# Performance work log

Hardware: AMD Instinct MI355X
Metric: run time of the kernel (lower is better)

The kernel has to match this reference:

```python
import jax, jax.numpy as jnp
import numpy as np

DIM = 512      # model dim
HEADS = 8      # attention heads
WS = 256       # window_size
G = 32         # num_global_tokens
SPARSITY = 0.3 # fraction of entries masked out per row by the sparsity controller


def setup_inputs() -> dict:
    key = jax.random.key(0)
    ks = jax.random.split(key, 7)
    b, n = 4, 8192
    x = jax.random.normal(ks[0], (b, n, DIM), dtype=jnp.float32)
    w_qkv = jax.random.normal(ks[1], (DIM, 3 * DIM), dtype=jnp.float32) * (DIM ** -0.5)
    w_out = jax.random.normal(ks[2], (DIM, DIM), dtype=jnp.float32) * (DIM ** -0.5)
    b_out = jnp.zeros((DIM,), dtype=jnp.float32)
    local_bias = jax.random.normal(ks[3], (HEADS, WS, WS), dtype=jnp.float32)
    global_param = jax.random.normal(ks[4], (HEADS, G, WS), dtype=jnp.float32)
    gate = jax.random.normal(ks[5], (HEADS,), dtype=jnp.float32)
    return {"x": x, "w_qkv": w_qkv, "w_out": w_out, "b_out": b_out,
            "local_bias": local_bias, "global_param": global_param, "gate": gate}


def reference(x, w_qkv, w_out, b_out, local_bias, global_param, gate):
    b, n, _ = x.shape
    h, ws, g = HEADS, WS, G
    d = DIM // h
    w = n // ws  # number of windows
    scale = DIM ** -0.5

    qkv = x @ w_qkv                      # [b, n, 3*dim]
    q, k, v = jnp.split(qkv, 3, axis=-1)

    def to_win(t):  # [b, n, dim] -> [b, h, w, ws, d]
        return t.reshape(b, n, h, d).transpose(0, 2, 1, 3).reshape(b, h, w, ws, d)

    q, k, v = to_win(q), to_win(k), to_win(v)

    # windowed local attention with learned per-window additive bias
    local = jnp.einsum('bhwnd,bhwmd->bhwnm', q, k) * scale   # [b,h,w,ws,ws]
    local = local + local_bias[None, :, None]                # bias broadcast over b, w

    # global-token attention term built from window-averaged q/k
    q_mean = q.mean(axis=2)  # [b,h,ws,d]
    k_mean = k.mean(axis=2)  # [b,h,ws,d]
    global_q = jnp.einsum('hgn,bhnd->bhgd', global_param, q_mean)      # [b,h,g,d]
    global_scores = jnp.einsum('bhgd,bhmd->bhgm', global_q, k_mean) * scale  # [b,h,g,ws]
    global_bias = global_scores.mean(axis=2)                            # [b,h,ws]

    # sparsity controller: learned per-head gate combines local + global,
    # then top-k row sparsification keeps (1-sparsity) of entries pre-softmax
    gate_h = jax.nn.sigmoid(gate)[None, :, None, None, None]
    scores = local + gate_h * global_bias[:, :, None, None, :]          # [b,h,w,ws,ws]
    k_keep = int(ws * (1.0 - SPARSITY))
    thresh = jax.lax.top_k(scores, k_keep)[0][..., -1:]                 # kth largest per row
    scores = jnp.where(scores >= thresh, scores, jnp.float32(-1e9))

    attn = jax.nn.softmax(scores, axis=-1)
    out = jnp.einsum('bhwnm,bhwmd->bhwnd', attn, v)                     # [b,h,w,ws,d]
    out = out.reshape(b, h, n, d).transpose(0, 2, 1, 3).reshape(b, n, DIM)
    return out @ w_out + b_out
```

## Files before the change

### kernel.cpp

```cpp
#include <hip/hip_runtime.h>

#define NN    8192
#define WSZ   256
#define KKEEP 179
#define SCALE 0.044194173824159216f

#define APLANE ((size_t)32768 * 512)
#define BPLANE ((size_t)1536 * 512)

typedef __attribute__((ext_vector_type(8))) __bf16 bf16x8;
typedef __attribute__((ext_vector_type(4))) short  s16x4;
typedef __attribute__((ext_vector_type(8))) short  s16x8;
typedef __attribute__((ext_vector_type(4))) float  f32x4;

struct Split3 { short h, m, l; };
__device__ __forceinline__ Split3 split3(float x)
{
    unsigned u  = __float_as_uint(x);
    unsigned hb = ((u + 0x7FFFu + ((u >> 16) & 1u)) >> 16) << 16;
    float r = x - __uint_as_float(hb);
    unsigned ur = __float_as_uint(r);
    unsigned mb = ((ur + 0x7FFFu + ((ur >> 16) & 1u)) >> 16) << 16;
    float r2 = r - __uint_as_float(mb);
    unsigned lr = __float_as_uint(r2);
    unsigned lb = (lr + 0x7FFFu + ((lr >> 16) & 1u)) >> 16;
    Split3 s;
    s.h = (short)(hb >> 16);
    s.m = (short)(mb >> 16);
    s.l = (short)(lb & 0xFFFFu);
    return s;
}

__device__ __forceinline__ void split2(float x, short& h, short& m)
{
    unsigned u  = __float_as_uint(x);
    unsigned hb = ((u + 0x7FFFu + ((u >> 16) & 1u)) >> 16) << 16;
    float r = x - __uint_as_float(hb);
    unsigned ur = __float_as_uint(r);
    unsigned mb = (ur + 0x7FFFu + ((ur >> 16) & 1u)) >> 16;
    h = (short)(hb >> 16);
    m = (short)(mb & 0xFFFFu);
}

__device__ __forceinline__ void async_copy16(short* dst_lds, const short* src)
{
    __builtin_amdgcn_global_load_lds(
        (const __attribute__((address_space(1))) void*)src,
        (__attribute__((address_space(3))) void*)dst_lds, 16, 0, 0);
}

__global__ __launch_bounds__(256) void splitw_kernel(const float* __restrict__ W,
                                                     int K, int N,
                                                     short* __restrict__ h,
                                                     short* __restrict__ m,
                                                     short* __restrict__ l)
{
    int idx = blockIdx.x * 256 + threadIdx.x;
    if (idx >= K * N) return;
    int k = idx / N, n = idx - k * N;
    Split3 s = split3(W[idx]);
    size_t o = (size_t)n * K + k;
    h[o] = s.h; m[o] = s.m; l[o] = s.l;
}

__global__ __launch_bounds__(256) void splitw_tiled(const float* __restrict__ W, int N,
                                                    short* __restrict__ Bh,
                                                    short* __restrict__ Bm,
                                                    short* __restrict__ Bl)
{
    __shared__ float raw[32 * 128];
    const int cb = blockIdx.x >> 4;
    const int kt = blockIdx.x & 15;
    const int t  = threadIdx.x;

#pragma unroll
    for (int l = 0; l < 4; ++l) {
        int f  = l * 256 + t;
        int k  = f >> 5;
        int nf = (f & 31) * 4;
        *(float4*)&raw[k * 128 + nf] =
            *(const float4*)&W[(size_t)(kt * 32 + k) * N + cb * 128 + nf];
    }
    __syncthreads();

    const int r  = t >> 1;
    const int hf = t & 1;
    const size_t base = ((size_t)(cb * 16 + kt) * 128 + r) * 32;
#pragma unroll
    for (int ss = 0; ss < 2; ++ss) {
        int s2 = hf * 2 + ss;
        s16x8 hv, mv, lv;
#pragma unroll
        for (int j = 0; j < 8; ++j) {
            Split3 sp = split3(raw[(s2 * 8 + j) * 128 + r]);
            hv[j] = sp.h; mv[j] = sp.m; lv[j] = sp.l;
        }
        size_t o = base + (size_t)((s2 ^ ((r >> 1) & 3)) << 3);
        *(s16x8*)&Bh[o] = hv;
        *(s16x8*)&Bm[o] = mv;
        *(s16x8*)&Bl[o] = lv;
    }
}

__global__ __launch_bounds__(256) void splitA_kernel(const float* __restrict__ X,
                                                     short* __restrict__ Ah,
                                                     short* __restrict__ Am,
                                                     short* __restrict__ Al)
{
    int idx = blockIdx.x * 256 + threadIdx.x;
    int row = idx >> 7;
    int kf  = (idx & 127) << 2;
    float4 a4 = *(const float4*)&X[((size_t)row << 9) + kf];
    int rb = row >> 7, r = row & 127;
    int kt = kf >> 5;
    int s  = (kf >> 3) & 3;
    int jj = kf & 7;
    size_t o = ((size_t)(rb * 16 + kt) * 128 + r) * 32
             + (size_t)((s ^ ((r >> 1) & 3)) << 3) + jj;
    Split3 s0 = split3(a4.x), s1 = split3(a4.y), s2 = split3(a4.z), s3 = split3(a4.w);
    s16x4 hv, mv, lv;
    hv[0] = s0.h; hv[1] = s1.h; hv[2] = s2.h; hv[3] = s3.h;
    mv[0] = s0.m; mv[1] = s1.m; mv[2] = s2.m; mv[3] = s3.m;
    lv[0] = s0.l; lv[1] = s1.l; lv[2] = s2.l; lv[3] = s3.l;
    *(s16x4*)&Ah[o] = hv;
    *(s16x4*)&Am[o] = mv;
    *(s16x4*)&Al[o] = lv;
}

__global__ __launch_bounds__(256, 3) void gemm_gload(const short* __restrict__ Ab,
                                                     const short* __restrict__ Bb,
                                                     float* __restrict__ C)
{
    __shared__ __align__(16) short S[6 * 4096];

    const int t    = threadIdx.x;
    const int lane = t & 63;
    const int wave = t >> 6;
    const int wr   = wave >> 1;
    const int wc   = wave & 1;
    const int fn   = lane & 15;
    const int slot = lane >> 4;
    const int rowBlk = blockIdx.y;
    const int colBlk = blockIdx.x;
    const int pstart = (colBlk < 8) ? 0 : 3;

    const int sa[6] = {2, 0, 1, 1, 0, 0};
    const int sb[6] = {0, 2, 1, 0, 1, 0};

    f32x4 acc[4][4] = {};

    for (int kt = 0; kt < 16; ++kt) {
        __syncthreads();
        const short* aT = Ab + ((size_t)(rowBlk * 16 + kt) << 12);
        const short* bT = Bb + ((size_t)(colBlk * 16 + kt) << 12);
#pragma unroll
        for (int c = 0; c < 12; ++c) {
            int g = wave * 12 + c;
            int p = g >> 3;
            int q = g & 7;
            const short* src = (p < 3 ? aT + (size_t)p * APLANE
                                      : bT + (size_t)(p - 3) * BPLANE)
                             + q * 512 + lane * 8;
            async_copy16(&S[g * 512], src);
        }
        __syncthreads();

        bf16x8 Bf[3][4];
#pragma unroll
        for (int s = 0; s < 3; ++s)
#pragma unroll
            for (int j = 0; j < 4; ++j) {
                int rowb = wc * 64 + j * 16 + fn;
                Bf[s][j] = *(const bf16x8*)&S[(3 + s) * 4096 + rowb * 32
                                              + ((slot ^ ((rowb >> 1) & 3)) << 3)];
            }

#pragma unroll
        for (int i = 0; i < 4; ++i) {
            int rowa = wr * 64 + i * 16 + fn;
            bf16x8 Af[3];
#pragma unroll
            for (int s = 0; s < 3; ++s)
                Af[s] = *(const bf16x8*)&S[s * 4096 + rowa * 32
                                           + ((slot ^ ((rowa >> 1) & 3)) << 3)];
#pragma unroll
            for (int p = 0; p < 6; ++p) {
                if (p < pstart) continue;
#pragma unroll
                for (int j = 0; j < 4; ++j)
                    acc[i][j] = __builtin_amdgcn_mfma_f32_16x16x32_bf16(
                        Af[sa[p]], Bf[sb[p]][j], acc[i][j], 0, 0, 0);
            }
        }
    }

    const int crow0 = rowBlk * 128 + wr * 64 + (lane >> 4) * 4;
    const int ccol0 = colBlk * 128 + wc * 64 + fn;
#pragma unroll
    for (int j = 0; j < 4; ++j) {
        int col = ccol0 + j * 16;
#pragma unroll
        for (int i = 0; i < 4; ++i)
#pragma unroll
            for (int r = 0; r < 4; ++r)
                C[(size_t)(crow0 + i * 16 + r) * 1536 + col] = acc[i][j][r];
    }
}

__global__ __launch_bounds__(256, 3) void gemm_mfma(const float* __restrict__ A, int lda,
                                                    const short* __restrict__ BTh,
                                                    const short* __restrict__ BTm,
                                                    const short* __restrict__ BTl,
                                                    const float* __restrict__ bias,
                                                    float* __restrict__ C, int ldc,
                                                    int qk_cols)
{
    __shared__ __align__(16) short Asm[3][128 * 32];
    __shared__ __align__(16) short Bsm[3][128 * 32];

    const int t       = threadIdx.x;
    const int lane    = t & 63;
    const int wave    = t >> 6;
    const int wr      = wave >> 1;
    const int wc      = wave & 1;
    const int rowBase = blockIdx.y * 128;
    const int colBase = blockIdx.x * 128;
    const int pstart  = (colBase < qk_cols) ? 0 : 3;

    const int sa[6] = {2, 0, 1, 1, 0, 0};
    const int sb[6] = {0, 2, 1, 0, 1, 0};

    const int fn   = lane & 15;
    const int slot = lane >> 4;

    f32x4 acc[4][4] = {};

    for (int ks = 0; ks < 512; ks += 32) {
        __syncthreads();

#pragma unroll
        for (int lo = 0; lo < 4; ++lo) {
            int idx = lo * 256 + t;
            int am  = idx >> 3;
            int af  = (idx & 7) * 4;
            float4 a4 = *(const float4*)&A[(size_t)(rowBase + am) * lda + ks + af];
            Split3 s0 = split3(a4.x);
            Split3 s1 = split3(a4.y);
            Split3 s2 = split3(a4.z);
            Split3 s3 = split3(a4.w);
            s16x4 hv, mv, lv;
            hv[0] = s0.h; hv[1] = s1.h; hv[2] = s2.h; hv[3] = s3.h;
            mv[0] = s0.m; mv[1] = s1.m; mv[2] = s2.m; mv[3] = s3.m;
            lv[0] = s0.l; lv[1] = s1.l; lv[2] = s2.l; lv[3] = s3.l;
            int o = am * 32 + (((af >> 3) ^ ((am >> 1) & 3)) << 3) + (af & 4);
            *(s16x4*)&Asm[0][o] = hv;
            *(s16x4*)&Asm[1][o] = mv;
            *(s16x4*)&Asm[2][o] = lv;
        }
#pragma unroll
        for (int lo = 0; lo < 2; ++lo) {
            int c = lo * 256 + t;
            int n = c >> 2;
            int q = (c & 3) * 8;
            size_t src = (size_t)(colBase + n) * 512 + ks + q;
            int o = n * 32 + (((q >> 3) ^ ((n >> 1) & 3)) << 3);
            *(s16x8*)&Bsm[0][o] = *(const s16x8*)&BTh[src];
            *(s16x8*)&Bsm[1][o] = *(const s16x8*)&BTm[src];
            *(s16x8*)&Bsm[2][o] = *(const s16x8*)&BTl[src];
        }
        __syncthreads();

        bf16x8 Bf[3][4];
#pragma unroll
        for (int s = 0; s < 3; ++s)
#pragma unroll
            for (int j = 0; j < 4; ++j) {
                int rowb = wc * 64 + j * 16 + fn;
                Bf[s][j] = *(const bf16x8*)&Bsm[s][rowb * 32
                                                   + ((slot ^ ((rowb >> 1) & 3)) << 3)];
            }

#pragma unroll
        for (int i = 0; i < 4; ++i) {
            int rowa = wr * 64 + i * 16 + fn;
            bf16x8 Af[3];
#pragma unroll
            for (int s = 0; s < 3; ++s)
                Af[s] = *(const bf16x8*)&Asm[s][rowa * 32
                                                + ((slot ^ ((rowa >> 1) & 3)) << 3)];
#pragma unroll
            for (int p = 0; p < 6; ++p) {
                if (p < pstart) continue;
#pragma unroll
                for (int j = 0; j < 4; ++j)
                    acc[i][j] = __builtin_amdgcn_mfma_f32_16x16x32_bf16(
                        Af[sa[p]], Bf[sb[p]][j], acc[i][j], 0, 0, 0);
            }
        }
    }

    const int crow0 = rowBase + wr * 64 + (lane >> 4) * 4;
    const int ccol0 = colBase + wc * 64 + fn;
#pragma unroll
    for (int j = 0; j < 4; ++j) {
        int col = ccol0 + j * 16;
        float bv = bias ? bias[col] : 0.0f;
#pragma unroll
        for (int i = 0; i < 4; ++i)
#pragma unroll
            for (int r = 0; r < 4; ++r)
                C[(size_t)(crow0 + i * 16 + r) * ldc + col] = acc[i][j][r] + bv;
    }
}

__global__ __launch_bounds__(256) void means_kernel(const float* __restrict__ qkv,
                                                    float* __restrict__ q_mean,
                                                    float* __restrict__ k_mean)
{
    int idx = blockIdx.x * 256 + threadIdx.x;
    int dd = idx & 63;
    int i  = (idx >> 6) & 255;
    int bh = idx >> 14;
    int b = bh >> 3, h = bh & 7;
    const float* base = qkv + (size_t)b * NN * 1536 + (size_t)h * 64 + dd;
    float qs = 0.f, ks = 0.f;
#pragma unroll
    for (int w = 0; w < 32; ++w) {
        size_t off = (size_t)(w * 256 + i) * 1536;
        qs += base[off];
        ks += base[off + 512];
    }
    q_mean[idx] = qs * 0.03125f;
    k_mean[idx] = ks * 0.03125f;
}

__global__ __launch_bounds__(256) void globalbias_kernel(const float* __restrict__ q_mean,
                                                         const float* __restrict__ k_mean,
                                                         const float* __restrict__ gp,
                                                         float* __restrict__ gbias)
{
    __shared__ float gq[32 * 64];
    const int bh = blockIdx.x;
    const int h  = bh & 7;
    const int t  = threadIdx.x;

#pragma unroll
    for (int e = 0; e < 8; ++e) {
        int idx = e * 256 + t;
        int g  = idx >> 6;
        int dd = idx & 63;
        const float* gpr = gp + (size_t)(h * 32 + g) * 256;
        const float* qm  = q_mean + (size_t)bh * 16384 + dd;
        float s = 0.f;
        for (int i = 0; i < 256; ++i) s += gpr[i] * qm[(size_t)i * 64];
        gq[idx] = s;
    }
    __syncthreads();

    const float* km = k_mean + (size_t)bh * 16384 + (size_t)t * 64;
    float4 kr[16];
#pragma unroll
    for (int j = 0; j < 16; ++j) kr[j] = *(const float4*)&km[4 * j];
    float acc = 0.f;
    for (int g = 0; g < 32; ++g) {
        const float* gqr = &gq[g * 64];
        float s = 0.f;
#pragma unroll
        for (int j = 0; j < 16; ++j) {
            float4 q4 = *(const float4*)&gqr[4 * j];
            s += q4.x * kr[j].x + q4.y * kr[j].y + q4.z * kr[j].z + q4.w * kr[j].w;
        }
        acc += s;
    }
    gbias[bh * 256 + t] = acc * SCALE * 0.03125f;
}

__device__ __forceinline__ unsigned mono_enc(float f) {
    unsigned u = __float_as_uint(f);
    return (u & 0x80000000u) ? ~u : (u | 0x80000000u);
}
__device__ __forceinline__ float mono_dec(unsigned e) {
    return (e & 0x80000000u) ? __uint_as_float(e ^ 0x80000000u)
                             : __uint_as_float(~e);
}

__global__ __launch_bounds__(256, 3) void attn_kernel(float* __restrict__ qkv,
                                                      const float* __restrict__ local_bias,
                                                      const float* __restrict__ gbias,
                                                      const float* __restrict__ gate)
{
    __shared__ __align__(16) short Qs[3 * 64 * 64];
    __shared__ __align__(16) short Ks[3 * 64 * 64];
    float* st = (float*)(void*)Ks;

    const int t    = threadIdx.x;
    const int lane = t & 63;
    const int wave = t >> 6;
    const int wr   = wave >> 1;
    const int wc   = wave & 1;
    const int fn   = lane & 15;
    const int fq   = (lane >> 4) * 8;
    const int g4   = (lane >> 4) * 4;

    const int blk = blockIdx.x;
    const int rc  = blk & 3;
    const int w   = (blk >> 2) & 31;
    const int bh  = blk >> 7;
    const int h   = bh & 7;
    const int b   = bh >> 3;
    const float gateh = 1.0f / (1.0f + __expf(-gate[h]));

    const size_t tokBase = (size_t)b * NN + (size_t)w * WSZ;
    float* qb = qkv + tokBase * 1536 + h * 64;
    const float* kb = qb + 512;
    const float* vb = qb + 1024;

    const int rr = t >> 2, sub = t & 3;

    const int sa[6] = {2, 0, 1, 1, 0, 0};
    const int sb[6] = {0, 2, 1, 0, 1, 0};

#pragma unroll
    for (int l = 0; l < 4; ++l) {
        int f  = l * 256 + t;
        int r  = f >> 4;
        int dg = (f & 15) * 4;
        float4 a4 = *(const float4*)&qb[(size_t)(rc * 64 + r) * 1536 + dg];
        Split3 s0 = split3(a4.x), s1 = split3(a4.y), s2 = split3(a4.z), s3 = split3(a4.w);
        s16x4 hv, mv, lv;
        hv[0] = s0.h; hv[1] = s1.h; hv[2] = s2.h; hv[3] = s3.h;
        mv[0] = s0.m; mv[1] = s1.m; mv[2] = s2.m; mv[3] = s3.m;
        lv[0] = s0.l; lv[1] = s1.l; lv[2] = s2.l; lv[3] = s3.l;
        int o = r * 64 + (dg ^ ((r & 7) << 3));
        *(s16x4*)&Qs[o]        = hv;
        *(s16x4*)&Qs[4096 + o] = mv;
        *(s16x4*)&Qs[8192 + o] = lv;
    }

    float vals[64];
#pragma unroll
    for (int mc = 0; mc < 4; ++mc) {
        __syncthreads();
#pragma unroll
        for (int l = 0; l < 4; ++l) {
            int f  = l * 256 + t;
            int m  = f >> 4;
            int dg = (f & 15) * 4;
            float4 a4 = *(const float4*)&kb[(size_t)(mc * 64 + m) * 1536 + dg];
            Split3 s0 = split3(a4.x), s1 = split3(a4.y), s2 = split3(a4.z), s3 = split3(a4.w);
            s16x4 hv, mv, lv;
            hv[0] = s0.h; hv[1] = s1.h; hv[2] = s2.h; hv[3] = s3.h;
            mv[0] = s0.m; mv[1] = s1.m; mv[2] = s2.m; mv[3] = s3.m;
            lv[0] = s0.l; lv[1] = s1.l; lv[2] = s2.l; lv[3] = s3.l;
            int o = m * 64 + (dg ^ ((m & 7) << 3));
            *(s16x4*)&Ks[o]        = hv;
            *(s16x4*)&Ks[4096 + o] = mv;
            *(s16x4*)&Ks[8192 + o] = lv;
        }
        __syncthreads();

        f32x4 acc[2][2] = {};
#pragma unroll
        for (int kk = 0; kk < 2; ++kk) {
            bf16x8 Af[3][2], Bf[3][2];
#pragma unroll
            for (int s = 0; s < 3; ++s)
#pragma unroll
                for (int i = 0; i < 2; ++i) {
                    int ar = wr * 32 + i * 16 + fn;
                    int bc = wc * 32 + i * 16 + fn;
                    Af[s][i] = *(const bf16x8*)&Qs[s * 4096 + ar * 64 + ((kk * 32 + fq) ^ ((ar & 7) << 3))];
                    Bf[s][i] = *(const bf16x8*)&Ks[s * 4096 + bc * 64 + ((kk * 32 + fq) ^ ((bc & 7) << 3))];
                }
#pragma unroll
            for (int p = 0; p < 6; ++p)
#pragma unroll
                for (int i = 0; i < 2; ++i)
#pragma unroll
                    for (int j = 0; j < 2; ++j)
                        acc[i][j] = __builtin_amdgcn_mfma_f32_16x16x32_bf16(
                            Af[sa[p]][i], Bf[sb[p]][j], acc[i][j], 0, 0, 0);
        }
        __syncthreads();

#pragma unroll
        for (int j = 0; j < 2; ++j) {
            int cl = wc * 32 + j * 16 + fn;
            int cf = mc * 64 + cl;
            float gb = gateh * gbias[bh * 256 + cf];
#pragma unroll
            for (int i = 0; i < 2; ++i)
#pragma unroll
                for (int r = 0; r < 4; ++r) {
                    int rl = wr * 32 + i * 16 + g4 + r;
                    st[rl * 68 + cl] = acc[i][j][r] * SCALE
                        + local_bias[((size_t)h * 256 + rc * 64 + rl) * 256 + cf] + gb;
                }
        }
        __syncthreads();
#pragma unroll
        for (int j = 0; j < 16; ++j)
            vals[mc * 16 + j] = st[rr * 68 + sub + 4 * j];
    }

    float rmin = vals[0], rmax = vals[0];
#pragma unroll
    for (int j = 1; j < 64; ++j) {
        rmin = fminf(rmin, vals[j]);
        rmax = fmaxf(rmax, vals[j]);
    }
    rmin = fminf(rmin, __shfl_xor(rmin, 1)); rmin = fminf(rmin, __shfl_xor(rmin, 2));
    rmax = fmaxf(rmax, __shfl_xor(rmax, 1)); rmax = fmaxf(rmax, __shfl_xor(rmax, 2));

    float flo = rmin, fhi = rmax;
    float thr = 0.f;
    bool  done = false;
    for (int it = 0; it < 16; ++it) {
        if (__all(done ? 1 : 0)) break;
        float mf = 0.5f * (flo + fhi);
        int c = 0;
#pragma unroll
        for (int j = 0; j < 64; ++j) c += (vals[j] >= mf) ? 1 : 0;
        c += __shfl_xor(c, 1);
        c += __shfl_xor(c, 2);
        if (!done) {
            if (c == KKEEP)      { thr = mf; done = true; }
            else if (c > KKEEP)  flo = mf;
            else                 fhi = mf;
        }
    }
    if (__any(done ? 0 : 1)) {
        unsigned lo_u = mono_enc(flo), hi_u = mono_enc(fhi);
        for (int it = 0; it < 34; ++it) {
            bool active = (!done) && (lo_u < hi_u);
            if (!__any(active ? 1 : 0)) break;
            unsigned span = hi_u - lo_u;
            unsigned mid  = lo_u + (span >> 1) + (span & 1u);
            float mf = mono_dec(mid);
            int c = 0;
#pragma unroll
            for (int j = 0; j < 64; ++j) c += (vals[j] >= mf) ? 1 : 0;
            c += __shfl_xor(c, 1);
            c += __shfl_xor(c, 2);
            if (active) {
                if (c == KKEEP)      { thr = mf; done = true; }
                else if (c >= KKEEP) lo_u = mid;
                else                 hi_u = mid - 1;
            }
        }
        if (!done) thr = mono_dec(lo_u);
    }

    float rmx = -3e38f;
#pragma unroll
    for (int j = 0; j < 64; ++j) rmx = fmaxf(rmx, (vals[j] >= thr) ? vals[j] : -3e38f);
    rmx = fmaxf(rmx, __shfl_xor(rmx, 1));
    rmx = fmaxf(rmx, __shfl_xor(rmx, 2));
    float rsum = 0.f;
#pragma unroll
    for (int j = 0; j < 64; ++j) {
        float e = (vals[j] >= thr) ? __expf(vals[j] - rmx) : 0.f;
        vals[j] = e;
        rsum += e;
    }
    rsum += __shfl_xor(rsum, 1);
    rsum += __shfl_xor(rsum, 2);
    float rinv = 1.0f / rsum;
#pragma unroll
    for (int j = 0; j < 64; ++j) vals[j] *= rinv;

    const int sa2[3] = {1, 0, 0};
    const int sb2[3] = {0, 1, 0};
    f32x4 acc2[2][2] = {};
#pragma unroll
    for (int mc = 0; mc < 4; ++mc) {
        __syncthreads();
#pragma unroll
        for (int u = 0; u < 16; ++u) {
            short ph, pm;
            split2(vals[mc * 16 + u], ph, pm);
            int ml   = sub + 4 * u;
            int slot = rr * 64 + (ml ^ ((rr & 7) << 3));
            Qs[slot]        = ph;
            Qs[4096 + slot] = pm;
        }
#pragma unroll
        for (int l = 0; l < 2; ++l) {
            int f  = l * 256 + t;
            int d  = f & 63;
            int mo = (f >> 6) * 8;
            s16x8 hv, mv;
#pragma unroll
            for (int i = 0; i < 8; ++i) {
                short vh, vm;
                split2(vb[(size_t)(mc * 64 + mo + i) * 1536 + d], vh, vm);
                hv[i] = vh; mv[i] = vm;
            }
            int o = d * 72 + mo;
            *(s16x8*)&Ks[o]        = hv;
            *(s16x8*)&Ks[4608 + o] = mv;
        }
        __syncthreads();

#pragma unroll
        for (int kk = 0; kk < 2; ++kk) {
            bf16x8 Pf[2][2], Vf[2][2];
#pragma unroll
            for (int s = 0; s < 2; ++s)
#pragma unroll
                for (int i = 0; i < 2; ++i) {
                    int pr = wr * 32 + i * 16 + fn;
                    int dr = wc * 32 + i * 16 + fn;
                    Pf[s][i] = *(const bf16x8*)&Qs[s * 4096 + pr * 64 + ((kk * 32 + fq) ^ ((pr & 7) << 3))];
                    Vf[s][i] = *(const bf16x8*)&Ks[s * 4608 + dr * 72 + kk * 32 + fq];
                }
#pragma unroll
            for (int p = 0; p < 3; ++p)
#pragma unroll
                for (int i = 0; i < 2; ++i)
#pragma unroll
                    for (int j = 0; j < 2; ++j)
                        acc2[i][j] = __builtin_amdgcn_mfma_f32_16x16x32_bf16(
                            Pf[sa2[p]][i], Vf[sb2[p]][j], acc2[i][j], 0, 0, 0);
        }
    }

#pragma unroll
    for (int j = 0; j < 2; ++j)
#pragma unroll
        for (int i = 0; i < 2; ++i)
#pragma unroll
            for (int r = 0; r < 4; ++r) {
                int row = rc * 64 + wr * 32 + i * 16 + g4 + r;
                int d   = wc * 32 + j * 16 + fn;
                qb[(size_t)row * 1536 + d] = acc2[i][j][r];
            }
}

extern "C" void kernel_launch(void* const* d_in, const int* in_sizes, int n_in,
                              void* d_out, int out_size, void* d_ws, size_t ws_size,
                              hipStream_t stream)
{
    (void)in_sizes; (void)n_in; (void)out_size;
    const float* x            = (const float*)d_in[0];
    const float* w_qkv        = (const float*)d_in[1];
    const float* w_out        = (const float*)d_in[2];
    const float* b_out        = (const float*)d_in[3];
    const float* local_bias   = (const float*)d_in[4];
    const float* global_param = (const float*)d_in[5];
    const float* gate         = (const float*)d_in[6];
    float* out = (float*)d_out;
    float* ws  = (float*)d_ws;

    float* qkv    = ws;
    float* q_mean = qkv + (size_t)32768 * 1536;
    float* k_mean = q_mean + (size_t)32 * 256 * 64;
    float* gb     = k_mean + (size_t)32 * 256 * 64;
    short* wsp    = (short*)(gb + 8192);
    short* WoTh = wsp;
    short* WoTm = WoTh + (size_t)512 * 512;
    short* WoTl = WoTm + (size_t)512 * 512;
    short* WqB  = WoTl + (size_t)512 * 512;
    short* Almb = WqB + 3 * BPLANE;

    size_t need = (size_t)((char*)(Almb + 3 * APLANE) - (char*)ws);
    bool pre = ws_size >= need;

    splitw_kernel<<<1024, 256, 0, stream>>>(w_out, 512, 512, WoTh, WoTm, WoTl);

    if (pre) {
        splitw_tiled<<<192, 256, 0, stream>>>(w_qkv, 1536,
                                              WqB, WqB + BPLANE, WqB + 2 * BPLANE);
        splitA_kernel<<<16384, 256, 0, stream>>>(x, Almb, Almb + APLANE, Almb + 2 * APLANE);
        gemm_gload<<<dim3(12, 256), 256, 0, stream>>>(Almb, WqB, qkv);
    } else {
        splitw_kernel<<<3072, 256, 0, stream>>>(w_qkv, 512, 1536,
                                                WqB, WqB + BPLANE, WqB + 2 * BPLANE);
        gemm_mfma<<<dim3(12, 256), 256, 0, stream>>>(x, 512, WqB, WqB + BPLANE,
                                                     WqB + 2 * BPLANE,
                                                     nullptr, qkv, 1536, 1024);
    }

    means_kernel<<<2048, 256, 0, stream>>>(qkv, q_mean, k_mean);
    globalbias_kernel<<<32, 256, 0, stream>>>(q_mean, k_mean, global_param, gb);
    attn_kernel<<<4096, 256, 0, stream>>>(qkv, local_bias, gb, gate);
    gemm_mfma<<<dim3(4, 256), 256, 0, stream>>>(qkv, 1536, WoTh, WoTm, WoTl,
                                                b_out, out, 512, 0);
}
```

Before: 692.0 us.

## Pipeline split-plane loads in gemm_gload and route output projection through it

The gemm_gload kernel now issues its async plane loads and waits with staged vmcnt counts, so MFMA work on the high-precision planes can start while the middle and low planes are still arriving. The A-split buffer is processed in row chunks sized to the available workspace. The output projection also moves to the pre-split gemm_gload path, using a 2-way split of the attention output instead of gemm_mfma's in-kernel conversion. This trades extra split kernel launches and global traffic for cheaper GEMM inner loops, and the 2-way split may slightly reduce accuracy on the output GEMM.

```diff
diff --git a/kernel.cpp b/kernel.cpp
--- a/kernel.cpp
+++ b/kernel.cpp
@@ -5,8 +5,8 @@
 #define KKEEP 179
 #define SCALE 0.044194173824159216f
 
-#define APLANE ((size_t)32768 * 512)
-#define BPLANE ((size_t)1536 * 512)
+#define BPLANE  ((size_t)1536 * 512)
+#define OPLANE  ((size_t)512 * 512)
 
 typedef __attribute__((ext_vector_type(8))) __bf16 bf16x8;
 typedef __attribute__((ext_vector_type(4))) short  s16x4;
@@ -49,6 +49,12 @@
         (__attribute__((address_space(3))) void*)dst_lds, 16, 0, 0);
 }
 
+__device__ __forceinline__ bf16x8 ldfrag(const short* S, int plane, int row, int slot)
+{
+    return *(const bf16x8*)&S[plane * 4096 + row * 32
+                              + ((slot ^ ((row >> 1) & 3)) << 3)];
+}
+
 __global__ __launch_bounds__(256) void splitw_kernel(const float* __restrict__ W,
                                                      int K, int N,
                                                      short* __restrict__ h,
@@ -102,15 +108,14 @@
     }
 }
 
-__global__ __launch_bounds__(256) void splitA_kernel(const float* __restrict__ X,
-                                                     short* __restrict__ Ah,
-                                                     short* __restrict__ Am,
-                                                     short* __restrict__ Al)
+__global__ __launch_bounds__(256) void splitA_kernel(const float* __restrict__ X, int lda,
+                                                     short* __restrict__ A0,
+                                                     size_t plane, int nsplit)
 {
     int idx = blockIdx.x * 256 + threadIdx.x;
     int row = idx >> 7;
     int kf  = (idx & 127) << 2;
-    float4 a4 = *(const float4*)&X[((size_t)row << 9) + kf];
+    float4 a4 = *(const float4*)&X[(size_t)row * lda + kf];
     int rb = row >> 7, r = row & 127;
     int kt = kf >> 5;
     int s  = (kf >> 3) & 3;
@@ -122,14 +127,18 @@
     hv[0] = s0.h; hv[1] = s1.h; hv[2] = s2.h; hv[3] = s3.h;
     mv[0] = s0.m; mv[1] = s1.m; mv[2] = s2.m; mv[3] = s3.m;
     lv[0] = s0.l; lv[1] = s1.l; lv[2] = s2.l; lv[3] = s3.l;
-    *(s16x4*)&Ah[o] = hv;
-    *(s16x4*)&Am[o] = mv;
-    *(s16x4*)&Al[o] = lv;
+    *(s16x4*)&A0[o]         = hv;
+    *(s16x4*)&A0[plane + o] = mv;
+    if (nsplit == 3) *(s16x4*)&A0[2 * plane + o] = lv;
 }
 
 __global__ __launch_bounds__(256, 3) void gemm_gload(const short* __restrict__ Ab,
+                                                     size_t aplane,
                                                      const short* __restrict__ Bb,
-                                                     float* __restrict__ C)
+                                                     size_t bplane,
+                                                     const float* __restrict__ bias,
+                                                     float* __restrict__ C, int ldc,
+                                                     int qkThresh)
 {
     __shared__ __align__(16) short S[6 * 4096];
 
@@ -142,54 +151,100 @@
     const int slot = lane >> 4;
     const int rowBlk = blockIdx.y;
     const int colBlk = blockIdx.x;
-    const int pstart = (colBlk < 8) ? 0 : 3;
-
-    const int sa[6] = {2, 0, 1, 1, 0, 0};
-    const int sb[6] = {0, 2, 1, 0, 1, 0};
+    const bool qk  = (colBlk < qkThresh);
 
     f32x4 acc[4][4] = {};
 
+    const int q0 = 2 * wave;
+
     for (int kt = 0; kt < 16; ++kt) {
-        __syncthreads();
+        asm volatile("s_barrier" ::: "memory");
+
         const short* aT = Ab + ((size_t)(rowBlk * 16 + kt) << 12);
         const short* bT = Bb + ((size_t)(colBlk * 16 + kt) << 12);
-#pragma unroll
-        for (int c = 0; c < 12; ++c) {
-            int g = wave * 12 + c;
-            int p = g >> 3;
-            int q = g & 7;
-            const short* src = (p < 3 ? aT + (size_t)p * APLANE
-                                      : bT + (size_t)(p - 3) * BPLANE)
-                             + q * 512 + lane * 8;
-            async_copy16(&S[g * 512], src);
-        }
-        __syncthreads();
-
-        bf16x8 Bf[3][4];
-#pragma unroll
-        for (int s = 0; s < 3; ++s)
-#pragma unroll
-            for (int j = 0; j < 4; ++j) {
-                int rowb = wc * 64 + j * 16 + fn;
-                Bf[s][j] = *(const bf16x8*)&S[(3 + s) * 4096 + rowb * 32
-                                              + ((slot ^ ((rowb >> 1) & 3)) << 3)];
-            }
-
-#pragma unroll
-        for (int i = 0; i < 4; ++i) {
-            int rowa = wr * 64 + i * 16 + fn;
-            bf16x8 Af[3];
-#pragma unroll
-            for (int s = 0; s < 3; ++s)
-                Af[s] = *(const bf16x8*)&S[s * 4096 + rowa * 32
-                                           + ((slot ^ ((rowa >> 1) & 3)) << 3)];
-#pragma unroll
-            for (int p = 0; p < 6; ++p) {
-                if (p < pstart) continue;
+
+        if (qk) {
+#pragma unroll
+            for (int s = 0; s < 3; ++s) {
+                async_copy16(&S[s * 4096 + q0 * 512],       aT + s * aplane + q0 * 512 + lane * 8);
+                async_copy16(&S[s * 4096 + (q0 + 1) * 512], aT + s * aplane + (q0 + 1) * 512 + lane * 8);
+                async_copy16(&S[(3 + s) * 4096 + q0 * 512],       bT + s * bplane + q0 * 512 + lane * 8);
+                async_copy16(&S[(3 + s) * 4096 + (q0 + 1) * 512], bT + s * bplane + (q0 + 1) * 512 + lane * 8);
+            }
+
+            asm volatile("s_waitcnt vmcnt(8)\n\ts_barrier" ::: "memory");
+            bf16x8 Bh[4], Bm[4], Bl[4];
+#pragma unroll
+            for (int j = 0; j < 4; ++j) Bh[j] = ldfrag(S, 3, wc * 64 + j * 16 + fn, slot);
+#pragma unroll
+            for (int i = 0; i < 4; ++i) {
+                bf16x8 Ah = ldfrag(S, 0, wr * 64 + i * 16 + fn, slot);
 #pragma unroll
                 for (int j = 0; j < 4; ++j)
-                    acc[i][j] = __builtin_amdgcn_mfma_f32_16x16x32_bf16(
-                        Af[sa[p]], Bf[sb[p]][j], acc[i][j], 0, 0, 0);
+                    acc[i][j] = __builtin_amdgcn_mfma_f32_16x16x32_bf16(Ah, Bh[j], acc[i][j], 0, 0, 0);
+            }
+
+            asm volatile("s_waitcnt vmcnt(4)\n\ts_barrier" ::: "memory");
+#pragma unroll
+            for (int j = 0; j < 4; ++j) Bm[j] = ldfrag(S, 4, wc * 64 + j * 16 + fn, slot);
+#pragma unroll
+            for (int i = 0; i < 4; ++i) {
+                bf16x8 Ah = ldfrag(S, 0, wr * 64 + i * 16 + fn, slot);
+                bf16x8 Am = ldfrag(S, 1, wr * 64 + i * 16 + fn, slot);
+#pragma unroll
+                for (int j = 0; j < 4; ++j) {
+                    acc[i][j] = __builtin_amdgcn_mfma_f32_16x16x32_bf16(Am, Bh[j], acc[i][j], 0, 0, 0);
+                    acc[i][j] = __builtin_amdgcn_mfma_f32_16x16x32_bf16(Ah, Bm[j], acc[i][j], 0, 0, 0);
+                    acc[i][j] = __builtin_amdgcn_mfma_f32_16x16x32_bf16(Am, Bm[j], acc[i][j], 0, 0, 0);
+                }
+            }
+
+            asm volatile("s_waitcnt vmcnt(0)\n\ts_barrier" ::: "memory");
+#pragma unroll
+            for (int j = 0; j < 4; ++j) Bl[j] = ldfrag(S, 5, wc * 64 + j * 16 + fn, slot);
+#pragma unroll
+            for (int i = 0; i < 4; ++i) {
+                bf16x8 Ah = ldfrag(S, 0, wr * 64 + i * 16 + fn, slot);
+                bf16x8 Al = ldfrag(S, 2, wr * 64 + i * 16 + fn, slot);
+#pragma unroll
+                for (int j = 0; j < 4; ++j) {
+                    acc[i][j] = __builtin_amdgcn_mfma_f32_16x16x32_bf16(Al, Bh[j], acc[i][j], 0, 0, 0);
+                    acc[i][j] = __builtin_amdgcn_mfma_f32_16x16x32_bf16(Ah, Bl[j], acc[i][j], 0, 0, 0);
+                }
+            }
+        } else {
+#pragma unroll
+            for (int s = 0; s < 2; ++s) {
+                async_copy16(&S[s * 4096 + q0 * 512],       aT + s * aplane + q0 * 512 + lane * 8);
+                async_copy16(&S[s * 4096 + (q0 + 1) * 512], aT + s * aplane + (q0 + 1) * 512 + lane * 8);
+                async_copy16(&S[(3 + s) * 4096 + q0 * 512],       bT + s * bplane + q0 * 512 + lane * 8);
+                async_copy16(&S[(3 + s) * 4096 + (q0 + 1) * 512], bT + s * bplane + (q0 + 1) * 512 + lane * 8);
+            }
+
+            asm volatile("s_waitcnt vmcnt(4)\n\ts_barrier" ::: "memory");
+            bf16x8 Bh[4], Bm[4];
+#pragma unroll
+            for (int j = 0; j < 4; ++j) Bh[j] = ldfrag(S, 3, wc * 64 + j * 16 + fn, slot);
+#pragma unroll
+            for (int i = 0; i < 4; ++i) {
+                bf16x8 Ah = ldfrag(S, 0, wr * 64 + i * 16 + fn, slot);
+#pragma unroll
+                for (int j = 0; j < 4; ++j)
+                    acc[i][j] = __builtin_amdgcn_mfma_f32_16x16x32_bf16(Ah, Bh[j], acc[i][j], 0, 0, 0);
+            }
+
+            asm volatile("s_waitcnt vmcnt(0)\n\ts_barrier" ::: "memory");
+#pragma unroll
+            for (int j = 0; j < 4; ++j) Bm[j] = ldfrag(S, 4, wc * 64 + j * 16 + fn, slot);
+#pragma unroll
+            for (int i = 0; i < 4; ++i) {
+                bf16x8 Ah = ldfrag(S, 0, wr * 64 + i * 16 + fn, slot);
+                bf16x8 Am = ldfrag(S, 1, wr * 64 + i * 16 + fn, slot);
+#pragma unroll
+                for (int j = 0; j < 4; ++j) {
+                    acc[i][j] = __builtin_amdgcn_mfma_f32_16x16x32_bf16(Am, Bh[j], acc[i][j], 0, 0, 0);
+                    acc[i][j] = __builtin_amdgcn_mfma_f32_16x16x32_bf16(Ah, Bm[j], acc[i][j], 0, 0, 0);
+                }
             }
         }
     }
@@ -199,11 +254,12 @@
 #pragma unroll
     for (int j = 0; j < 4; ++j) {
         int col = ccol0 + j * 16;
+        float bv = bias ? bias[col] : 0.0f;
 #pragma unroll
         for (int i = 0; i < 4; ++i)
 #pragma unroll
             for (int r = 0; r < 4; ++r)
-                C[(size_t)(crow0 + i * 16 + r) * 1536 + col] = acc[i][j][r];
+                C[(size_t)(crow0 + i * 16 + r) * ldc + col] = acc[i][j][r] + bv;
     }
 }
 
@@ -656,24 +712,31 @@
     float* q_mean = qkv + (size_t)32768 * 1536;
     float* k_mean = q_mean + (size_t)32 * 256 * 64;
     float* gb     = k_mean + (size_t)32 * 256 * 64;
-    short* wsp    = (short*)(gb + 8192);
-    short* WoTh = wsp;
-    short* WoTm = WoTh + (size_t)512 * 512;
-    short* WoTl = WoTm + (size_t)512 * 512;
-    short* WqB  = WoTl + (size_t)512 * 512;
-    short* Almb = WqB + 3 * BPLANE;
-
-    size_t need = (size_t)((char*)(Almb + 3 * APLANE) - (char*)ws);
-    bool pre = ws_size >= need;
-
-    splitw_kernel<<<1024, 256, 0, stream>>>(w_out, 512, 512, WoTh, WoTm, WoTl);
+    short* WoB    = (short*)(gb + 8192);
+    short* WqB    = WoB + 3 * OPLANE;
+    short* Achk   = WqB + 3 * BPLANE;
+
+    size_t used  = (size_t)((char*)Achk - (char*)ws);
+    size_t avail = ws_size > used ? ws_size - used : 0;
+    int C = 32768;
+    while (C >= 4096 && (size_t)3 * C * 512 * 2 > avail) C >>= 1;
+    bool pre = (C >= 4096);
 
     if (pre) {
+        size_t aplane = (size_t)C * 512;
         splitw_tiled<<<192, 256, 0, stream>>>(w_qkv, 1536,
                                               WqB, WqB + BPLANE, WqB + 2 * BPLANE);
-        splitA_kernel<<<16384, 256, 0, stream>>>(x, Almb, Almb + APLANE, Almb + 2 * APLANE);
-        gemm_gload<<<dim3(12, 256), 256, 0, stream>>>(Almb, WqB, qkv);
+        splitw_tiled<<<64, 256, 0, stream>>>(w_out, 512,
+                                             WoB, WoB + OPLANE, WoB + 2 * OPLANE);
+        for (int r0 = 0; r0 < 32768; r0 += C) {
+            splitA_kernel<<<C / 2, 256, 0, stream>>>(x + (size_t)r0 * 512, 512,
+                                                     Achk, aplane, 3);
+            gemm_gload<<<dim3(12, C / 128), 256, 0, stream>>>(
+                Achk, aplane, WqB, BPLANE, nullptr, qkv + (size_t)r0 * 1536, 1536, 8);
+        }
     } else {
+        splitw_kernel<<<1024, 256, 0, stream>>>(w_out, 512, 512,
+                                                WoB, WoB + OPLANE, WoB + 2 * OPLANE);
         splitw_kernel<<<3072, 256, 0, stream>>>(w_qkv, 512, 1536,
                                                 WqB, WqB + BPLANE, WqB + 2 * BPLANE);
         gemm_mfma<<<dim3(12, 256), 256, 0, stream>>>(x, 512, WqB, WqB + BPLANE,
@@ -684,6 +747,18 @@
     means_kernel<<<2048, 256, 0, stream>>>(qkv, q_mean, k_mean);
     globalbias_kernel<<<32, 256, 0, stream>>>(q_mean, k_mean, global_param, gb);
     attn_kernel<<<4096, 256, 0, stream>>>(qkv, local_bias, gb, gate);
-    gemm_mfma<<<dim3(4, 256), 256, 0, stream>>>(qkv, 1536, WoTh, WoTm, WoTl,
-                                                b_out, out, 512, 0);
-}
+
+    if (pre) {
+        size_t aplane = (size_t)C * 512;
+        for (int r0 = 0; r0 < 32768; r0 += C) {
+            splitA_kernel<<<C / 2, 256, 0, stream>>>(qkv + (size_t)r0 * 1536, 1536,
+                                                     Achk, aplane, 2);
+            gemm_gload<<<dim3(4, C / 128), 256, 0, stream>>>(
+                Achk, aplane, WoB, OPLANE, b_out, out + (size_t)r0 * 512, 512, 0);
+        }
+    } else {
+        gemm_mfma<<<dim3(4, 256), 256, 0, stream>>>(qkv, 1536, WoB, WoB + OPLANE,
+                                                    WoB + 2 * OPLANE,
+                                                    b_out, out, 512, 0);
+    }
+}
```

After: 973.9 us. 40.7% more time.
